# Performance work log

Hardware: AMD Instinct MI355X
Metric: run time of the kernel (lower is better)

Reference implementation:

```python
import jax, jax.numpy as jnp
import numpy as np

H = 16      # query heads
G = 4       # kv heads
D = 64      # head dim
ROPE_BASE = 10000.0

def _rotate_half(t):
    t1, t2 = jnp.split(t, 2, axis=-1)
    return jnp.concatenate([-t2, t1], axis=-1)

def _rope_emb(n):
    inv_freq = 1.0 / (ROPE_BASE ** (jnp.arange(0, D, 2, dtype=jnp.float32) / D))
    freqs = jnp.outer(jnp.arange(n, dtype=jnp.float32), inv_freq)  # [n, D/2]
    return jnp.concatenate([freqs, freqs], axis=-1)               # [n, D]

def setup_inputs() -> dict:
    key = jax.random.key(0)
    k1, k2, k3, k4 = jax.random.split(key, 4)
    B, N, C = 2, 2048, 1024
    x = jax.random.normal(k1, (B, N, C), dtype=jnp.float32)
    w_q = jax.random.normal(k2, (C, C), dtype=jnp.float32) * 0.02
    w_kv = jax.random.normal(k3, (C, 2 * G * D), dtype=jnp.float32) * 0.02
    w_out = jax.random.normal(k4, (C, C), dtype=jnp.float32) * 0.02
    return {"x": x, "w_q": w_q, "w_kv": w_kv, "w_out": w_out}

def reference(x, w_q, w_kv, w_out):
    B, N, C = x.shape
    scale = D ** -0.5
    q = (x @ w_q).reshape(B, N, H, D).transpose(0, 2, 1, 3)        # [B,H,N,D]
    kv = x @ w_kv
    k, v = jnp.split(kv, 2, axis=-1)
    k = k.reshape(B, N, G, D).transpose(0, 2, 1, 3)                # [B,G,N,D]
    v = v.reshape(B, N, G, D).transpose(0, 2, 1, 3)
    emb = _rope_emb(N)                                             # [N,D]
    cos, sin = jnp.cos(emb), jnp.sin(emb)
    q = q * cos + _rotate_half(q) * sin
    k = k * cos + _rotate_half(k) * sin
    # NOTE: faithful to source einsum -- kv-head axis g is SUMMED (absent from output)
    scores = jnp.einsum('bhid,bgjd->bhij', q, k) * scale           # [B,H,N,N]
    probs = jax.nn.softmax(scores, axis=-1)
    out = jnp.einsum('bhij,bgjd->bhid', probs, v)                  # [B,H,N,D]
    out = out.transpose(0, 2, 1, 3).reshape(B, N, H * D)
    return out @ w_out
```

## Files before the change

### kernel.cpp

```cpp
#include <hip/hip_runtime.h>
#include <hip/hip_bf16.h>
#include <math.h>

#define B_ 2
#define N_ 2048
#define C_ 1024
#define H_ 16
#define G_ 4
#define D_ 64
#define QKV_N 1152

using short8  = __attribute__((ext_vector_type(8))) short;
using short4v = __attribute__((ext_vector_type(4))) short;
using float4v = __attribute__((ext_vector_type(4))) float;

#if __has_builtin(__builtin_amdgcn_mfma_f32_16x16x16_bf16)
#define MFMA16K16(A, B, C) __builtin_amdgcn_mfma_f32_16x16x16_bf16(A, B, C, 0, 0, 0)
#else
#define MFMA16K16(A, B, C) __builtin_amdgcn_mfma_f32_16x16x16bf16_1k(A, B, C, 0, 0, 0)
#endif

__device__ __forceinline__ ushort f2bf(float f) {
    union { float f; unsigned u; } v; v.f = f;
    unsigned r = (v.u + 0x7FFF + ((v.u >> 16) & 1)) >> 16;
    return (ushort)r;
}
__device__ __forceinline__ float bf2f(ushort u) {
    union { unsigned u; float f; } t; t.u = ((unsigned)u) << 16; return t.f;
}
__device__ __forceinline__ unsigned pack_bf16(float a, float b) {
#if __has_builtin(__builtin_amdgcn_cvt_pk_bf16_f32)
    auto t = __builtin_amdgcn_cvt_pk_bf16_f32(a, b);
    unsigned r; __builtin_memcpy(&r, &t, 4); return r;
#else
    return (unsigned)f2bf(a) | ((unsigned)f2bf(b) << 16);
#endif
}
__device__ __forceinline__ float fexp2(float x) {
#if __has_builtin(__builtin_amdgcn_exp2f)
    return __builtin_amdgcn_exp2f(x);
#else
    return exp2f(x);
#endif
}

__device__ void tconv_body(const float* __restrict__ src, ushort* __restrict__ dst,
                           int K, int N, int bx, int by, float (*T)[65]) {
    const int n0 = bx * 64, k0 = by * 64;
    const int tid = threadIdx.x;
    #pragma unroll
    for (int s = 0; s < 16; ++s) {
        int idx = tid + s * 256; int r = idx >> 6, cc = idx & 63;
        T[r][cc] = src[(size_t)(k0 + r) * N + n0 + cc];
    }
    __syncthreads();
    #pragma unroll
    for (int s = 0; s < 16; ++s) {
        int idx = tid + s * 256; int r = idx >> 6, cc = idx & 63;
        dst[(size_t)(n0 + r) * K + k0 + cc] = f2bf(T[cc][r]);
    }
}

__global__ void prep(const float* __restrict__ x, const float* __restrict__ w_q,
                     const float* __restrict__ w_kv, const float* __restrict__ w_out,
                     ushort* __restrict__ xb, ushort* __restrict__ wqkvT,
                     ushort* __restrict__ woutT) {
    __shared__ float T[64][65];
    const int blk = blockIdx.x, tid = threadIdx.x;
    if (blk < 4096) {
        int i = blk * 1024 + tid * 4;
        float4 v = *(const float4*)(x + i);
        ushort4 o;
        o.x = f2bf(v.x); o.y = f2bf(v.y); o.z = f2bf(v.z); o.w = f2bf(v.w);
        *(ushort4*)(xb + i) = o;
    } else if (blk < 4352) {
        int idx = blk - 4096;
        tconv_body(w_q, wqkvT, C_, C_, idx & 15, idx >> 4, T);
    } else if (blk < 4608) {
        int idx = blk - 4352;
        tconv_body(w_out, woutT, C_, C_, idx & 15, idx >> 4, T);
    } else {
        const int k0 = (blk - 4608) * 64;
        #pragma unroll
        for (int it = 0; it < 4; ++it) {
            int p = tid + it * 256;
            int kk = p >> 4, d4 = (p & 15) * 4;
            float ks[4] = {0, 0, 0, 0}, vs[4] = {0, 0, 0, 0};
            #pragma unroll
            for (int g = 0; g < G_; ++g) {
                float4 a = *(const float4*)(w_kv + (size_t)(k0 + kk) * 512 + g * 64 + d4);
                float4 b = *(const float4*)(w_kv + (size_t)(k0 + kk) * 512 + 256 + g * 64 + d4);
                ks[0] += a.x; ks[1] += a.y; ks[2] += a.z; ks[3] += a.w;
                vs[0] += b.x; vs[1] += b.y; vs[2] += b.z; vs[3] += b.w;
            }
            #pragma unroll
            for (int e = 0; e < 4; ++e) {
                wqkvT[(size_t)(1024 + d4 + e) * C_ + k0 + kk] = f2bf(ks[e]);
                wqkvT[(size_t)(1088 + d4 + e) * C_ + k0 + kk] = f2bf(vs[e]);
            }
        }
    }
}

template <bool F32OUT>
__global__ __launch_bounds__(256, 4) void gemm128(const ushort* __restrict__ A,
                                                  const ushort* __restrict__ Bt,
                                                  void* __restrict__ Cv,
                                                  int M, int N, int K) {
    __shared__ __align__(16) ushort As[128 * 64];
    __shared__ __align__(16) ushort Bs[64 * 64];

    const int tid = threadIdx.x, wave = tid >> 6, lane = tid & 63;
    const int g = lane >> 4, c = lane & 15;
    const int m0 = blockIdx.y * 128, n0 = blockIdx.x * 64;

    const int lr = tid >> 3;
    const int lq = tid & 7;
    const int gsw = (lq ^ (lr & 7)) * 8;
    const ushort* pa = A  + (size_t)(m0 + lr) * K + gsw;
    const ushort* pb = Bt + (size_t)(n0 + lr) * K + gsw;

    float4v acc[2][4];
    #pragma unroll
    for (int m = 0; m < 2; ++m)
        #pragma unroll
        for (int n = 0; n < 4; ++n) acc[m][n] = {0, 0, 0, 0};

    for (int k0 = 0; k0 < K; k0 += 64) {
        #pragma unroll
        for (int i = 0; i < 4; ++i)
            __builtin_amdgcn_global_load_lds(
                (const __attribute__((address_space(1))) void*)(pa + (size_t)i * 32 * K + k0),
                (__attribute__((address_space(3))) void*)&As[(i * 32 + wave * 8) * 64], 16, 0, 0);
        #pragma unroll
        for (int i = 0; i < 2; ++i)
            __builtin_amdgcn_global_load_lds(
                (const __attribute__((address_space(1))) void*)(pb + (size_t)i * 32 * K + k0),
                (__attribute__((address_space(3))) void*)&Bs[(i * 32 + wave * 8) * 64], 16, 0, 0);
        __syncthreads();

        #pragma unroll
        for (int kk = 0; kk < 2; ++kk) {
            const int c7 = c & 7;
            short8 af[2], bf[4];
            #pragma unroll
            for (int m = 0; m < 2; ++m)
                af[m] = *(const short8*)&As[(wave * 32 + m * 16 + c) * 64 + ((kk * 4 + g) ^ c7) * 8];
            #pragma unroll
            for (int n = 0; n < 4; ++n)
                bf[n] = *(const short8*)&Bs[(n * 16 + c) * 64 + ((kk * 4 + g) ^ c7) * 8];
            #pragma unroll
            for (int m = 0; m < 2; ++m)
                #pragma unroll
                for (int n = 0; n < 4; ++n)
                    acc[m][n] = __builtin_amdgcn_mfma_f32_16x16x32_bf16(af[m], bf[n], acc[m][n], 0, 0, 0);
        }
        __syncthreads();
    }

    #pragma unroll
    for (int m = 0; m < 2; ++m)
        #pragma unroll
        for (int n = 0; n < 4; ++n)
            #pragma unroll
            for (int r = 0; r < 4; ++r) {
                int rowi = m0 + wave * 32 + m * 16 + 4 * g + r;
                int coli = n0 + n * 16 + c;
                if (F32OUT) ((float*)Cv)[(size_t)rowi * N + coli] = acc[m][n][r];
                else ((ushort*)Cv)[(size_t)rowi * N + coli] = f2bf(acc[m][n][r]);
            }
}

__global__ void rope_kv(const ushort* __restrict__ qkvb,
                        ushort* __restrict__ Kt, ushort* __restrict__ VtT) {
    const int wid = threadIdx.x >> 6, d = threadIdx.x & 63;
    const int rowg = blockIdx.x * 4 + wid;
    const int n = rowg & (N_ - 1), b = rowg >> 11;

    const ushort* base = qkvb + (size_t)rowg * QKV_N + 1024;
    float ks = bf2f(base[d]);
    float partner = __shfl_xor(ks, 32, 64);
    float rh = (d < 32) ? -partner : partner;
    float ang = (float)n * __powf(10000.0f, -(float)(d & 31) * (1.0f / 32.0f));
    float sn, cs; __sincosf(ang, &sn, &cs);

    Kt[(size_t)rowg * 64 + d] = f2bf(ks * cs + rh * sn);
    VtT[((size_t)b * 64 + d) * N_ + n] = base[64 + d];
}

#define QSCALE 0.18033688011112042f

__global__ __launch_bounds__(256, 4) void attn10(
        const ushort* __restrict__ qkvb, const ushort* __restrict__ Kt,
        const ushort* __restrict__ VtT,
        ushort* __restrict__ oP0, ushort* __restrict__ oP1,
        float* __restrict__ lP0, float* __restrict__ lP1) {
    const int s  = blockIdx.x & 1;
    const int qt = (blockIdx.x >> 1) & 15;
    const int h  = (blockIdx.x >> 5) & 15;
    const int b  = blockIdx.x >> 9;
    const int tid = threadIdx.x, wave = tid >> 6, lane = tid & 63;
    const int g = lane >> 4, c = lane & 15;

    __shared__ __align__(16) ushort Ksh[64 * 64];
    __shared__ __align__(16) ushort Vsh[64 * 64];

    ushort* oPs = s ? oP1 : oP0;
    float*  lPs = s ? lP1 : lP0;

    const int i0 = qt * 128 + wave * 32;
    float invf[8];
    #pragma unroll
    for (int i = 0; i < 8; ++i)
        invf[i] = __powf(10000.0f, -(float)(8 * g + i) * (1.0f / 32.0f));

    short8 qf[2][2];
    #pragma unroll
    for (int a = 0; a < 2; ++a) {
        const int row = i0 + a * 16 + c;
        const ushort* qrow = qkvb + (size_t)(b * N_ + row) * QKV_N + h * 64;
        short8 raw0 = *(const short8*)(qrow + 8 * g);
        short8 raw1 = *(const short8*)(qrow + 32 + 8 * g);
        #pragma unroll
        for (int i = 0; i < 8; ++i) {
            float f0 = bf2f((ushort)raw0[i]), f1 = bf2f((ushort)raw1[i]);
            float sn, cs; __sincosf((float)row * invf[i], &sn, &cs);
            qf[a][0][i] = (short)f2bf((f0 * cs - f1 * sn) * QSCALE);
            qf[a][1][i] = (short)f2bf((f1 * cs + f0 * sn) * QSCALE);
        }
    }

    float4v o[2][4];
    #pragma unroll
    for (int a = 0; a < 2; ++a)
        #pragma unroll
        for (int f = 0; f < 4; ++f) o[a][f] = {0, 0, 0, 0};
    float ll[2] = {0.f, 0.f};

    const ushort* Kb = Kt  + (size_t)b * N_ * 64;
    const ushort* Vb = VtT + (size_t)b * 64 * N_;
    const int lr8 = lane >> 3, lq8 = lane & 7;
    const int wpos = (lq8 ^ lr8) * 8;
    const int j0 = s * (N_ / 2);
    const int NT = (N_ / 2) / 64;

    short8 kr0 = *(const short8*)(Kb + (size_t)(j0 + wave * 16 + lr8) * 64 + lq8 * 8);
    short8 kr1 = *(const short8*)(Kb + (size_t)(j0 + wave * 16 + 8 + lr8) * 64 + lq8 * 8);
    short8 vr0 = *(const short8*)(Vb + (size_t)(wave * 16 + lr8) * N_ + j0 + lq8 * 8);
    short8 vr1 = *(const short8*)(Vb + (size_t)(wave * 16 + 8 + lr8) * N_ + j0 + lq8 * 8);

    for (int t = 0; t < NT; ++t) {
        __syncthreads();
        *(short8*)&Ksh[(wave * 16 + lr8) * 64 + wpos]     = kr0;
        *(short8*)&Ksh[(wave * 16 + 8 + lr8) * 64 + wpos] = kr1;
        *(short8*)&Vsh[(wave * 16 + lr8) * 64 + wpos]     = vr0;
        *(short8*)&Vsh[(wave * 16 + 8 + lr8) * 64 + wpos] = vr1;
        __syncthreads();
        if (t + 1 < NT) {
            const int jn = j0 + (t + 1) * 64;
            kr0 = *(const short8*)(Kb + (size_t)(jn + wave * 16 + lr8) * 64 + lq8 * 8);
            kr1 = *(const short8*)(Kb + (size_t)(jn + wave * 16 + 8 + lr8) * 64 + lq8 * 8);
            vr0 = *(const short8*)(Vb + (size_t)(wave * 16 + lr8) * N_ + jn + lq8 * 8);
            vr1 = *(const short8*)(Vb + (size_t)(wave * 16 + 8 + lr8) * N_ + jn + lq8 * 8);
        }

        #pragma unroll
        for (int jt4 = 0; jt4 < 4; ++jt4) {
            const int R = jt4 * 16 + c;
            short8 kf0 = *(const short8*)&Ksh[R * 64 + ((g ^ (c & 7)) * 8)];
            short8 kf1 = *(const short8*)&Ksh[R * 64 + (((g ^ 4) ^ (c & 7)) * 8)];
            short4v vf[4];
            #pragma unroll
            for (int f = 0; f < 4; ++f)
                vf[f] = *(const short4v*)&Vsh[(16 * f + c) * 64 +
                          (((jt4 * 2 + (g >> 1)) ^ (c & 7)) * 8) + (g & 1) * 4];

            #pragma unroll
            for (int a = 0; a < 2; ++a) {
                float4v st = {0, 0, 0, 0};
                st = __builtin_amdgcn_mfma_f32_16x16x32_bf16(kf0, qf[a][0], st, 0, 0, 0);
                st = __builtin_amdgcn_mfma_f32_16x16x32_bf16(kf1, qf[a][1], st, 0, 0, 0);
                float p0 = fexp2(st[0]), p1 = fexp2(st[1]);
                float p2 = fexp2(st[2]), p3 = fexp2(st[3]);
                ll[a] += (p0 + p1) + (p2 + p3);
                union { unsigned u[2]; short4v v; } pk;
                pk.u[0] = pack_bf16(p0, p1);
                pk.u[1] = pack_bf16(p2, p3);
                #pragma unroll
                for (int f = 0; f < 4; ++f)
                    o[a][f] = MFMA16K16(vf[f], pk.v, o[a][f]);
            }
        }
    }

    #pragma unroll
    for (int a = 0; a < 2; ++a) {
        float lt = ll[a];
        lt += __shfl_xor(lt, 16, 64);
        lt += __shfl_xor(lt, 32, 64);
        const int row = i0 + a * 16 + c;
        if (g == 0) lPs[(size_t)(b * N_ + row) * 16 + h] = lt;
        #pragma unroll
        for (int f = 0; f < 4; ++f) {
            ushort4 w;
            w.x = f2bf(o[a][f][0]); w.y = f2bf(o[a][f][1]);
            w.z = f2bf(o[a][f][2]); w.w = f2bf(o[a][f][3]);
            *(ushort4*)(oPs + (size_t)(b * N_ + row) * 1024 + h * 64 + 16 * f + 4 * g) = w;
        }
    }
}

__global__ void combine(const ushort* __restrict__ oP0, const ushort* __restrict__ oP1,
                        const float* __restrict__ lP0, const float* __restrict__ lP1,
                        ushort* __restrict__ ao) {
    const int e = (blockIdx.x * 256 + threadIdx.x) * 4;
    const int row = e >> 10, hh = (e >> 6) & 15;
    const float inv = 1.0f / (lP0[row * 16 + hh] + lP1[row * 16 + hh]);
    ushort4 a = *(const ushort4*)(oP0 + e);
    ushort4 b = *(const ushort4*)(oP1 + e);
    ushort4 r;
    r.x = f2bf((bf2f(a.x) + bf2f(b.x)) * inv);
    r.y = f2bf((bf2f(a.y) + bf2f(b.y)) * inv);
    r.z = f2bf((bf2f(a.z) + bf2f(b.z)) * inv);
    r.w = f2bf((bf2f(a.w) + bf2f(b.w)) * inv);
    *(ushort4*)(ao + e) = r;
}

extern "C" void kernel_launch(void* const* d_in, const int* in_sizes, int n_in,
                              void* d_out, int out_size, void* d_ws, size_t ws_size,
                              hipStream_t stream) {
    const float* x     = (const float*)d_in[0];
    const float* w_q   = (const float*)d_in[1];
    const float* w_kv  = (const float*)d_in[2];
    const float* w_out = (const float*)d_in[3];
    float* out = (float*)d_out;

    const int M = B_ * N_;
    ushort* xb    = (ushort*)d_ws;
    ushort* wqkvT = xb    + (size_t)M * C_;
    ushort* woutT = wqkvT + (size_t)QKV_N * C_;
    ushort* qkvb  = woutT + (size_t)C_ * C_;
    ushort* Kt    = qkvb  + (size_t)M * QKV_N;
    ushort* VtT   = Kt    + (size_t)B_ * N_ * D_;
    ushort* oP1   = VtT   + (size_t)B_ * D_ * N_;
    float*  lP0   = (float*)(oP1 + (size_t)M * C_);
    float*  lP1   = lP0 + (size_t)M * H_;
    ushort* oP0   = xb;
    ushort* ao    = xb;

    prep<<<4624, 256, 0, stream>>>(x, w_q, w_kv, w_out, xb, wqkvT, woutT);
    gemm128<false><<<dim3(QKV_N / 64, M / 128), 256, 0, stream>>>(xb, wqkvT, qkvb, M, QKV_N, C_);
    rope_kv<<<M / 4, 256, 0, stream>>>(qkvb, Kt, VtT);
    attn10<<<B_ * H_ * (N_ / 128) * 2, 256, 0, stream>>>(qkvb, Kt, VtT, oP0, oP1, lP0, lP1);
    combine<<<(M * C_) / 1024, 256, 0, stream>>>(oP0, oP1, lP0, lP1, ao);
    gemm128<true><<<dim3(C_ / 64, M / 128), 256, 0, stream>>>(ao, woutT, out, M, C_, C_);
}
```

Measured before the change: 190.1 us.

## Double-buffer GEMM, fuse RoPE/V-transpose into QKV epilogue, 4-way KV split attention

The GEMM now double-buffers its LDS tiles so the next K-slab's global→LDS copy overlaps the current MFMAs. The QKV GEMM epilogue applies RoPE to K and writes the transposed V directly, which removes the separate rope_kv kernel and its extra global traffic. Attention moves to 256-query tiles, each wave handling 64 rows, and splits the key range four ways instead of two, with a four-input combine. This adds register pressure in attention, twice the LDS in the GEMM, and more partial-output traffic in combine.

```diff
diff --git a/kernel.cpp b/kernel.cpp
--- a/kernel.cpp
+++ b/kernel.cpp
@@ -102,13 +102,15 @@
     }
 }
 
-template <bool F32OUT>
-__global__ __launch_bounds__(256, 4) void gemm128(const ushort* __restrict__ A,
-                                                  const ushort* __restrict__ Bt,
-                                                  void* __restrict__ Cv,
-                                                  int M, int N, int K) {
-    __shared__ __align__(16) ushort As[128 * 64];
-    __shared__ __align__(16) ushort Bs[64 * 64];
+template <int MODE>
+__global__ __launch_bounds__(256) void gemm128p(const ushort* __restrict__ A,
+                                                const ushort* __restrict__ Bt,
+                                                void* __restrict__ Cv,
+                                                ushort* __restrict__ Kt,
+                                                ushort* __restrict__ VtT,
+                                                int M, int N, int K) {
+    __shared__ __align__(16) ushort As[2][128 * 64];
+    __shared__ __align__(16) ushort Bs[2][64 * 64];
 
     const int tid = threadIdx.x, wave = tid >> 6, lane = tid & 63;
     const int g = lane >> 4, c = lane & 15;
@@ -120,24 +122,32 @@
     const ushort* pa = A  + (size_t)(m0 + lr) * K + gsw;
     const ushort* pb = Bt + (size_t)(n0 + lr) * K + gsw;
 
-    float4v acc[2][4];
-    #pragma unroll
-    for (int m = 0; m < 2; ++m)
-        #pragma unroll
-        for (int n = 0; n < 4; ++n) acc[m][n] = {0, 0, 0, 0};
-
-    for (int k0 = 0; k0 < K; k0 += 64) {
+    auto stage = [&](int buf, int k0) {
         #pragma unroll
         for (int i = 0; i < 4; ++i)
             __builtin_amdgcn_global_load_lds(
                 (const __attribute__((address_space(1))) void*)(pa + (size_t)i * 32 * K + k0),
-                (__attribute__((address_space(3))) void*)&As[(i * 32 + wave * 8) * 64], 16, 0, 0);
+                (__attribute__((address_space(3))) void*)&As[buf][(i * 32 + wave * 8) * 64], 16, 0, 0);
         #pragma unroll
         for (int i = 0; i < 2; ++i)
             __builtin_amdgcn_global_load_lds(
                 (const __attribute__((address_space(1))) void*)(pb + (size_t)i * 32 * K + k0),
-                (__attribute__((address_space(3))) void*)&Bs[(i * 32 + wave * 8) * 64], 16, 0, 0);
-        __syncthreads();
+                (__attribute__((address_space(3))) void*)&Bs[buf][(i * 32 + wave * 8) * 64], 16, 0, 0);
+    };
+
+    float4v acc[2][4];
+    #pragma unroll
+    for (int m = 0; m < 2; ++m)
+        #pragma unroll
+        for (int n = 0; n < 4; ++n) acc[m][n] = {0, 0, 0, 0};
+
+    stage(0, 0);
+    __syncthreads();
+
+    const int NT = K >> 6;
+    int cur = 0;
+    for (int t = 0; t < NT; ++t) {
+        if (t + 1 < NT) stage(cur ^ 1, (t + 1) << 6);
 
         #pragma unroll
         for (int kk = 0; kk < 2; ++kk) {
@@ -145,10 +155,10 @@
             short8 af[2], bf[4];
             #pragma unroll
             for (int m = 0; m < 2; ++m)
-                af[m] = *(const short8*)&As[(wave * 32 + m * 16 + c) * 64 + ((kk * 4 + g) ^ c7) * 8];
+                af[m] = *(const short8*)&As[cur][(wave * 32 + m * 16 + c) * 64 + ((kk * 4 + g) ^ c7) * 8];
             #pragma unroll
             for (int n = 0; n < 4; ++n)
-                bf[n] = *(const short8*)&Bs[(n * 16 + c) * 64 + ((kk * 4 + g) ^ c7) * 8];
+                bf[n] = *(const short8*)&Bs[cur][(n * 16 + c) * 64 + ((kk * 4 + g) ^ c7) * 8];
             #pragma unroll
             for (int m = 0; m < 2; ++m)
                 #pragma unroll
@@ -156,6 +166,44 @@
                     acc[m][n] = __builtin_amdgcn_mfma_f32_16x16x32_bf16(af[m], bf[n], acc[m][n], 0, 0, 0);
         }
         __syncthreads();
+        cur ^= 1;
+    }
+
+    if (MODE == 1 && blockIdx.x >= 16) {
+        if (blockIdx.x == 16) {
+            const float invf_e = __powf(10000.0f, -(float)c * (1.0f / 32.0f));
+            const float invf_o = __powf(10000.0f, -(float)(c + 16) * (1.0f / 32.0f));
+            #pragma unroll
+            for (int m = 0; m < 2; ++m)
+                #pragma unroll
+                for (int r = 0; r < 4; ++r) {
+                    const int rowi = m0 + wave * 32 + m * 16 + 4 * g + r;
+                    const float nf = (float)(rowi & (N_ - 1));
+                    float sn0, cs0, sn1, cs1;
+                    __sincosf(nf * invf_e, &sn0, &cs0);
+                    __sincosf(nf * invf_o, &sn1, &cs1);
+                    #pragma unroll
+                    for (int nn = 0; nn < 4; ++nn) {
+                        const float v = acc[m][nn][r], p = acc[m][nn ^ 2][r];
+                        const float rh = (nn < 2) ? -p : p;
+                        const float sn = (nn & 1) ? sn1 : sn0;
+                        const float cs = (nn & 1) ? cs1 : cs0;
+                        Kt[(size_t)rowi * 64 + nn * 16 + c] = f2bf(v * cs + rh * sn);
+                    }
+                }
+        } else {
+            #pragma unroll
+            for (int m = 0; m < 2; ++m)
+                #pragma unroll
+                for (int nn = 0; nn < 4; ++nn)
+                    #pragma unroll
+                    for (int r = 0; r < 4; ++r) {
+                        const int rowi = m0 + wave * 32 + m * 16 + 4 * g + r;
+                        const int n = rowi & (N_ - 1), bb = rowi >> 11;
+                        VtT[((size_t)bb * 64 + nn * 16 + c) * N_ + n] = f2bf(acc[m][nn][r]);
+                    }
+        }
+        return;
     }
 
     #pragma unroll
@@ -166,37 +214,21 @@
             for (int r = 0; r < 4; ++r) {
                 int rowi = m0 + wave * 32 + m * 16 + 4 * g + r;
                 int coli = n0 + n * 16 + c;
-                if (F32OUT) ((float*)Cv)[(size_t)rowi * N + coli] = acc[m][n][r];
+                if (MODE == 2) ((float*)Cv)[(size_t)rowi * N + coli] = acc[m][n][r];
                 else ((ushort*)Cv)[(size_t)rowi * N + coli] = f2bf(acc[m][n][r]);
             }
 }
 
-__global__ void rope_kv(const ushort* __restrict__ qkvb,
-                        ushort* __restrict__ Kt, ushort* __restrict__ VtT) {
-    const int wid = threadIdx.x >> 6, d = threadIdx.x & 63;
-    const int rowg = blockIdx.x * 4 + wid;
-    const int n = rowg & (N_ - 1), b = rowg >> 11;
-
-    const ushort* base = qkvb + (size_t)rowg * QKV_N + 1024;
-    float ks = bf2f(base[d]);
-    float partner = __shfl_xor(ks, 32, 64);
-    float rh = (d < 32) ? -partner : partner;
-    float ang = (float)n * __powf(10000.0f, -(float)(d & 31) * (1.0f / 32.0f));
-    float sn, cs; __sincosf(ang, &sn, &cs);
-
-    Kt[(size_t)rowg * 64 + d] = f2bf(ks * cs + rh * sn);
-    VtT[((size_t)b * 64 + d) * N_ + n] = base[64 + d];
-}
-
 #define QSCALE 0.18033688011112042f
 
-__global__ __launch_bounds__(256, 4) void attn10(
+__global__ __launch_bounds__(256, 4) void attn13(
         const ushort* __restrict__ qkvb, const ushort* __restrict__ Kt,
         const ushort* __restrict__ VtT,
         ushort* __restrict__ oP0, ushort* __restrict__ oP1,
-        float* __restrict__ lP0, float* __restrict__ lP1) {
-    const int s  = blockIdx.x & 1;
-    const int qt = (blockIdx.x >> 1) & 15;
+        ushort* __restrict__ oP2, ushort* __restrict__ oP3,
+        float* __restrict__ lP) {
+    const int s  = blockIdx.x & 3;
+    const int qt = (blockIdx.x >> 2) & 7;
     const int h  = (blockIdx.x >> 5) & 15;
     const int b  = blockIdx.x >> 9;
     const int tid = threadIdx.x, wave = tid >> 6, lane = tid & 63;
@@ -205,18 +237,17 @@
     __shared__ __align__(16) ushort Ksh[64 * 64];
     __shared__ __align__(16) ushort Vsh[64 * 64];
 
-    ushort* oPs = s ? oP1 : oP0;
-    float*  lPs = s ? lP1 : lP0;
-
-    const int i0 = qt * 128 + wave * 32;
+    ushort* oPs = (s == 0) ? oP0 : (s == 1) ? oP1 : (s == 2) ? oP2 : oP3;
+
+    const int i0 = qt * 256 + wave * 64;
     float invf[8];
     #pragma unroll
     for (int i = 0; i < 8; ++i)
         invf[i] = __powf(10000.0f, -(float)(8 * g + i) * (1.0f / 32.0f));
 
-    short8 qf[2][2];
-    #pragma unroll
-    for (int a = 0; a < 2; ++a) {
+    short8 qf[4][2];
+    #pragma unroll
+    for (int a = 0; a < 4; ++a) {
         const int row = i0 + a * 16 + c;
         const ushort* qrow = qkvb + (size_t)(b * N_ + row) * QKV_N + h * 64;
         short8 raw0 = *(const short8*)(qrow + 8 * g);
@@ -230,19 +261,19 @@
         }
     }
 
-    float4v o[2][4];
-    #pragma unroll
-    for (int a = 0; a < 2; ++a)
+    float4v o[4][4];
+    #pragma unroll
+    for (int a = 0; a < 4; ++a)
         #pragma unroll
         for (int f = 0; f < 4; ++f) o[a][f] = {0, 0, 0, 0};
-    float ll[2] = {0.f, 0.f};
+    float ll[4] = {0.f, 0.f, 0.f, 0.f};
 
     const ushort* Kb = Kt  + (size_t)b * N_ * 64;
     const ushort* Vb = VtT + (size_t)b * 64 * N_;
     const int lr8 = lane >> 3, lq8 = lane & 7;
     const int wpos = (lq8 ^ lr8) * 8;
-    const int j0 = s * (N_ / 2);
-    const int NT = (N_ / 2) / 64;
+    const int j0 = s * (N_ / 4);
+    const int NT = (N_ / 4) / 64;
 
     short8 kr0 = *(const short8*)(Kb + (size_t)(j0 + wave * 16 + lr8) * 64 + lq8 * 8);
     short8 kr1 = *(const short8*)(Kb + (size_t)(j0 + wave * 16 + 8 + lr8) * 64 + lq8 * 8);
@@ -276,7 +307,7 @@
                           (((jt4 * 2 + (g >> 1)) ^ (c & 7)) * 8) + (g & 1) * 4];
 
             #pragma unroll
-            for (int a = 0; a < 2; ++a) {
+            for (int a = 0; a < 4; ++a) {
                 float4v st = {0, 0, 0, 0};
                 st = __builtin_amdgcn_mfma_f32_16x16x32_bf16(kf0, qf[a][0], st, 0, 0, 0);
                 st = __builtin_amdgcn_mfma_f32_16x16x32_bf16(kf1, qf[a][1], st, 0, 0, 0);
@@ -294,12 +325,12 @@
     }
 
     #pragma unroll
-    for (int a = 0; a < 2; ++a) {
+    for (int a = 0; a < 4; ++a) {
         float lt = ll[a];
         lt += __shfl_xor(lt, 16, 64);
         lt += __shfl_xor(lt, 32, 64);
         const int row = i0 + a * 16 + c;
-        if (g == 0) lPs[(size_t)(b * N_ + row) * 16 + h] = lt;
+        if (g == 0) lP[((size_t)s * (B_ * N_) + b * N_ + row) * 16 + h] = lt;
         #pragma unroll
         for (int f = 0; f < 4; ++f) {
             ushort4 w;
@@ -310,19 +341,23 @@
     }
 }
 
-__global__ void combine(const ushort* __restrict__ oP0, const ushort* __restrict__ oP1,
-                        const float* __restrict__ lP0, const float* __restrict__ lP1,
-                        ushort* __restrict__ ao) {
+__global__ void combine4(const ushort* __restrict__ oP0, const ushort* __restrict__ oP1,
+                         const ushort* __restrict__ oP2, const ushort* __restrict__ oP3,
+                         const float* __restrict__ lP, ushort* __restrict__ ao) {
     const int e = (blockIdx.x * 256 + threadIdx.x) * 4;
     const int row = e >> 10, hh = (e >> 6) & 15;
-    const float inv = 1.0f / (lP0[row * 16 + hh] + lP1[row * 16 + hh]);
+    const size_t MH = (size_t)B_ * N_ * 16;
+    const float inv = 1.0f / (lP[row * 16 + hh] + lP[MH + row * 16 + hh] +
+                              lP[2 * MH + row * 16 + hh] + lP[3 * MH + row * 16 + hh]);
     ushort4 a = *(const ushort4*)(oP0 + e);
     ushort4 b = *(const ushort4*)(oP1 + e);
+    ushort4 cc = *(const ushort4*)(oP2 + e);
+    ushort4 d = *(const ushort4*)(oP3 + e);
     ushort4 r;
-    r.x = f2bf((bf2f(a.x) + bf2f(b.x)) * inv);
-    r.y = f2bf((bf2f(a.y) + bf2f(b.y)) * inv);
-    r.z = f2bf((bf2f(a.z) + bf2f(b.z)) * inv);
-    r.w = f2bf((bf2f(a.w) + bf2f(b.w)) * inv);
+    r.x = f2bf((bf2f(a.x) + bf2f(b.x) + bf2f(cc.x) + bf2f(d.x)) * inv);
+    r.y = f2bf((bf2f(a.y) + bf2f(b.y) + bf2f(cc.y) + bf2f(d.y)) * inv);
+    r.z = f2bf((bf2f(a.z) + bf2f(b.z) + bf2f(cc.z) + bf2f(d.z)) * inv);
+    r.w = f2bf((bf2f(a.w) + bf2f(b.w) + bf2f(cc.w) + bf2f(d.w)) * inv);
     *(ushort4*)(ao + e) = r;
 }
 
@@ -343,15 +378,15 @@
     ushort* Kt    = qkvb  + (size_t)M * QKV_N;
     ushort* VtT   = Kt    + (size_t)B_ * N_ * D_;
     ushort* oP1   = VtT   + (size_t)B_ * D_ * N_;
-    float*  lP0   = (float*)(oP1 + (size_t)M * C_);
-    float*  lP1   = lP0 + (size_t)M * H_;
+    ushort* oP2   = oP1   + (size_t)M * C_;
+    ushort* oP3   = oP2   + (size_t)M * C_;
+    float*  lP    = (float*)(oP3 + (size_t)M * C_);
     ushort* oP0   = xb;
     ushort* ao    = xb;
 
     prep<<<4624, 256, 0, stream>>>(x, w_q, w_kv, w_out, xb, wqkvT, woutT);
-    gemm128<false><<<dim3(QKV_N / 64, M / 128), 256, 0, stream>>>(xb, wqkvT, qkvb, M, QKV_N, C_);
-    rope_kv<<<M / 4, 256, 0, stream>>>(qkvb, Kt, VtT);
-    attn10<<<B_ * H_ * (N_ / 128) * 2, 256, 0, stream>>>(qkvb, Kt, VtT, oP0, oP1, lP0, lP1);
-    combine<<<(M * C_) / 1024, 256, 0, stream>>>(oP0, oP1, lP0, lP1, ao);
-    gemm128<true><<<dim3(C_ / 64, M / 128), 256, 0, stream>>>(ao, woutT, out, M, C_, C_);
-}
+    gemm128p<1><<<dim3(QKV_N / 64, M / 128), 256, 0, stream>>>(xb, wqkvT, qkvb, Kt, VtT, M, QKV_N, C_);
+    attn13<<<B_ * H_ * (N_ / 256) * 4, 256, 0, stream>>>(qkvb, Kt, VtT, oP0, oP1, oP2, oP3, lP);
+    combine4<<<(M * C_) / 1024, 256, 0, stream>>>(oP0, oP1, oP2, oP3, lP, ao);
+    gemm128p<2><<<dim3(C_ / 64, M / 128), 256, 0, stream>>>(ao, woutT, out, nullptr, nullptr, M, C_, C_);
+}
```

New measurement: 657.4 us. 246% more time.
